# Optimization experiments

Measured on AMD Instinct MI355X. Metric: run time of the kernel, lower is better.

## Reference

```python
import jax, jax.numpy as jnp
import numpy as np
from jax import lax


def _fuse_proj(proj):
    # proj: [B,2,4,4] -> [B,4,4]; K @ [R|t] into top 3x4 of extrinsics
    p = proj[:, 0]
    new34 = jnp.einsum('bij,bjk->bik', proj[:, 1, :3, :3], proj[:, 0, :3, :4])
    return p.at[:, :3, :4].set(new34)


def _homo_warp(src_fea, src_proj, ref_proj, depth_values):
    # src_fea [B,C,H,W], src_proj/ref_proj [B,4,4], depth_values [B,D]
    B, C, H, W = src_fea.shape
    D = depth_values.shape[1]
    proj = jnp.einsum('bij,bjk->bik', src_proj, jnp.linalg.inv(ref_proj))
    rot, trans = proj[:, :3, :3], proj[:, :3, 3:4]
    y, x = jnp.meshgrid(jnp.arange(H, dtype=src_fea.dtype),
                        jnp.arange(W, dtype=src_fea.dtype), indexing='ij')
    xyz = jnp.stack([x.ravel(), y.ravel(), jnp.ones(H * W, src_fea.dtype)])  # [3,HW]
    rot_xyz = jnp.einsum('bij,jk->bik', rot, xyz)                            # [B,3,HW]
    pxyz = rot_xyz[:, :, None, :] * depth_values[:, None, :, None] + trans[:, :, None, :]  # [B,3,D,HW]
    z = pxyz[:, 2]
    px = pxyz[:, 0] / z   # pixel coords (align_corners=True convention)
    py = pxyz[:, 1] / z
    # bilinear sample with zeros padding
    x0 = jnp.floor(px); y0 = jnp.floor(py)
    x1 = x0 + 1.0;      y1 = y0 + 1.0
    wx1 = px - x0; wx0 = 1.0 - wx1
    wy1 = py - y0; wy0 = 1.0 - wy1
    fea_flat = src_fea.reshape(B, C, H * W)

    def corner(xc, yc, w):
        valid = (xc >= 0) & (xc <= W - 1) & (yc >= 0) & (yc <= H - 1)
        idx = (jnp.clip(yc, 0, H - 1).astype(jnp.int32) * W
               + jnp.clip(xc, 0, W - 1).astype(jnp.int32)).reshape(B, -1)   # [B,D*HW]
        g = jax.vmap(lambda f, i: jnp.take(f, i, axis=1))(fea_flat, idx)    # [B,C,D*HW]
        return g * (w * valid.astype(w.dtype)).reshape(B, 1, -1)

    out = (corner(x0, y0, wx0 * wy0) + corner(x1, y0, wx1 * wy0)
           + corner(x0, y1, wx0 * wy1) + corner(x1, y1, wx1 * wy1))
    return out.reshape(B, C, D, H, W)


def _forward(features, proj_matrices, depth_values, reg_w, num_depth):
    N = features.shape[0]
    ref_fea = features[0]                      # [B,C,H,W]
    ref_proj = _fuse_proj(proj_matrices[:, 0])
    B, C, H, W = ref_fea.shape
    D = num_depth

    vol_sum = jnp.broadcast_to(ref_fea[:, :, None], (B, C, D, H, W))
    vol_sq = vol_sum ** 2
    for i in range(1, N):                      # small fixed view loop
        src_proj = _fuse_proj(proj_matrices[:, i])
        wv = _homo_warp(features[i], src_proj, ref_proj, depth_values)
        vol_sum = vol_sum + wv
        vol_sq = vol_sq + wv ** 2
    inv_n = 1.0 / N
    variance = vol_sq * inv_n - (vol_sum * inv_n) ** 2   # [B,C,D,H,W]

    # cost regularization: 3x3x3 conv C->1 (stand-in for external 3D CNN)
    cost = lax.conv_general_dilated(variance, reg_w, (1, 1, 1), 'SAME',
                                    dimension_numbers=('NCDHW', 'OIDHW', 'NCDHW'))[:, 0]  # [B,D,H,W]
    prob = jax.nn.softmax(cost, axis=1)
    depth = jnp.sum(prob * depth_values[:, :, None, None], axis=1)          # [B,H,W]

    # photometric confidence (no-grad block)
    p = lax.stop_gradient(prob)
    # 4*avg_pool3d(pad(prob,(1,2)) over depth, kernel (4,1,1)) == sliding sum of 4
    sum4 = lax.reduce_window(p, 0.0, lax.add, (1, 4, 1, 1), (1, 1, 1, 1),
                             ((0, 0), (1, 2), (0, 0), (0, 0)))
    didx = jnp.sum(p * jnp.arange(D, dtype=p.dtype)[None, :, None, None], axis=1)
    didx = jnp.clip(didx.astype(jnp.int32), 0, D - 1)                        # [B,H,W]
    conf = jnp.take_along_axis(sum4, didx[:, None], axis=1)[:, 0]            # [B,H,W]
    return depth, conf


def setup_inputs() -> dict:
    key = jax.random.key(0)
    k1, k2, k3 = jax.random.split(key, 3)
    N, B, C, H, W, D = 5, 1, 32, 128, 160, 48
    features = jax.random.normal(k1, (N, B, C, H, W), jnp.float32)
    eye = jnp.eye(4, dtype=jnp.float32)
    proj_matrices = eye + 0.01 * jax.random.normal(k2, (B, N, 2, 4, 4), jnp.float32)
    depth_values = jnp.broadcast_to(
        425.0 + 510.0 * jnp.arange(D, dtype=jnp.float32) / (D - 1), (B, D))
    reg_w = 0.05 * jax.random.normal(k3, (1, C, 3, 3, 3), jnp.float32)
    return {"features": features, "proj_matrices": proj_matrices,
            "depth_values": depth_values, "reg_w": reg_w, "num_depth": D}


def reference(features, proj_matrices, depth_values, reg_w, num_depth):
    return _forward(features, proj_matrices, depth_values, reg_w, num_depth)
```

## Files before the change

kernel.cpp:

```cpp
#include <hip/hip_runtime.h>

#define W_ 160
#define H_ 128
#define C_ 32
#define D_ 48
#define HW_ (H_*W_)
#define TX 16
#define TY 16
#define HPX 18
#define HPY 18
#define NHP (HPX*HPY)
#define NHPP 336
#define NT 21
#define DST 28

typedef _Float16 h8 __attribute__((ext_vector_type(8)));
typedef __fp16 fp16x2 __attribute__((ext_vector_type(2)));
typedef float f4 __attribute__((ext_vector_type(4)));

__device__ __forceinline__ _Float16 u2h(unsigned int u) {
    union { unsigned short s; _Float16 h; } x; x.s = (unsigned short)u; return x.h;
}
__device__ __forceinline__ unsigned int pkh2(float a, float b) {
    union { fp16x2 h; unsigned int u; } x;
    x.h = __builtin_amdgcn_cvt_pkrtz(a, b);
    return x.u;
}

__device__ __forceinline__ void inv4x4(const float* a, float* inv) {
    inv[0]  =  a[5]*a[10]*a[15] - a[5]*a[11]*a[14] - a[9]*a[6]*a[15] + a[9]*a[7]*a[14] + a[13]*a[6]*a[11] - a[13]*a[7]*a[10];
    inv[4]  = -a[4]*a[10]*a[15] + a[4]*a[11]*a[14] + a[8]*a[6]*a[15] - a[8]*a[7]*a[14] - a[12]*a[6]*a[11] + a[12]*a[7]*a[10];
    inv[8]  =  a[4]*a[9]*a[15]  - a[4]*a[11]*a[13] - a[8]*a[5]*a[15] + a[8]*a[7]*a[13] + a[12]*a[5]*a[11] - a[12]*a[7]*a[9];
    inv[12] = -a[4]*a[9]*a[14]  + a[4]*a[10]*a[13] + a[8]*a[5]*a[14] - a[8]*a[6]*a[13] - a[12]*a[5]*a[10] + a[12]*a[6]*a[9];
    inv[1]  = -a[1]*a[10]*a[15] + a[1]*a[11]*a[14] + a[9]*a[2]*a[15] - a[9]*a[3]*a[14] - a[13]*a[2]*a[11] + a[13]*a[3]*a[10];
    inv[5]  =  a[0]*a[10]*a[15] - a[0]*a[11]*a[14] - a[8]*a[2]*a[15] + a[8]*a[3]*a[14] + a[12]*a[2]*a[11] - a[12]*a[3]*a[10];
    inv[9]  = -a[0]*a[9]*a[15]  + a[0]*a[11]*a[13] + a[8]*a[1]*a[15] - a[8]*a[3]*a[13] - a[12]*a[1]*a[11] + a[12]*a[3]*a[9];
    inv[13] =  a[0]*a[9]*a[14]  - a[0]*a[10]*a[13] - a[8]*a[1]*a[14] + a[8]*a[2]*a[13] + a[12]*a[1]*a[10] - a[12]*a[2]*a[9];
    inv[2]  =  a[1]*a[6]*a[15]  - a[1]*a[7]*a[14]  - a[5]*a[2]*a[15] + a[5]*a[3]*a[14] + a[13]*a[2]*a[7]  - a[13]*a[3]*a[6];
    inv[6]  = -a[0]*a[6]*a[15]  + a[0]*a[7]*a[14]  + a[4]*a[2]*a[15] - a[4]*a[3]*a[14] - a[12]*a[2]*a[7]  + a[12]*a[3]*a[6];
    inv[10] =  a[0]*a[5]*a[15]  - a[0]*a[7]*a[13]  - a[4]*a[1]*a[15] + a[4]*a[3]*a[13] + a[12]*a[1]*a[7]  - a[12]*a[3]*a[5];
    inv[14] = -a[0]*a[5]*a[14]  + a[0]*a[6]*a[13]  + a[4]*a[1]*a[14] - a[4]*a[2]*a[13] - a[12]*a[1]*a[6]  + a[12]*a[2]*a[5];
    inv[3]  = -a[1]*a[6]*a[11]  + a[1]*a[7]*a[10]  + a[5]*a[2]*a[11] - a[5]*a[3]*a[10] - a[9]*a[2]*a[7]   + a[9]*a[3]*a[6];
    inv[7]  =  a[0]*a[6]*a[11]  - a[0]*a[7]*a[10]  - a[4]*a[2]*a[11] + a[4]*a[3]*a[10] + a[8]*a[2]*a[7]   - a[8]*a[3]*a[6];
    inv[11] = -a[0]*a[5]*a[11]  + a[0]*a[7]*a[9]   + a[4]*a[1]*a[11] - a[4]*a[3]*a[9]  - a[8]*a[1]*a[7]   + a[8]*a[3]*a[5];
    inv[15] =  a[0]*a[5]*a[10]  - a[0]*a[6]*a[9]   - a[4]*a[1]*a[10] + a[4]*a[2]*a[9]  + a[8]*a[1]*a[6]   - a[8]*a[2]*a[5];
    float det = a[0]*inv[0] + a[1]*inv[4] + a[2]*inv[8] + a[3]*inv[12];
    float id = 1.0f / det;
    for (int i = 0; i < 16; ++i) inv[i] *= id;
}

__device__ __forceinline__ void fuseProj(const float* proj, int i, float* F) {
    const float* A = proj + i*32;
    const float* R = A + 16;
    for (int r = 0; r < 3; ++r)
        for (int k = 0; k < 4; ++k)
            F[r*4+k] = R[r*4]*A[k] + R[r*4+1]*A[4+k] + R[r*4+2]*A[8+k];
    for (int k = 0; k < 4; ++k) F[12+k] = A[12+k];
}

__global__ __launch_bounds__(256) void kS(const float* __restrict__ f,
                                          const float* __restrict__ proj,
                                          _Float16* __restrict__ ft,
                                          float* __restrict__ RX,
                                          float* __restrict__ M) {
    __shared__ float t[64][33];
    const int bx = blockIdx.x, v = blockIdx.y;
    const int tid = threadIdx.x;
    if (bx < 320) {
        const int p0 = bx * 64;
        const int pl = tid & 63;
        const int cb = (tid >> 6) * 8;
        #pragma unroll
        for (int k = 0; k < 8; ++k)
            t[pl][cb + k] = f[(size_t)(v*C_ + cb + k)*HW_ + p0 + pl];
        __syncthreads();
        const int px = tid >> 2;
        const int c0 = (tid & 3) * 8;
        h8 o;
        #pragma unroll
        for (int k = 0; k < 8; ++k) o[k] = (_Float16)t[px][c0 + k];
        *(h8*)&ft[((size_t)(v*HW_ + p0 + px) << 5) + c0] = o;
    } else {
        if (v >= 4) return;
        float F0[16], Fv[16], inv[16], P[12];
        fuseProj(proj, 0, F0);
        fuseProj(proj, v + 1, Fv);
        inv4x4(F0, inv);
        #pragma unroll
        for (int r = 0; r < 3; ++r)
            #pragma unroll
            for (int c = 0; c < 4; ++c) {
                float acc = 0.f;
                #pragma unroll
                for (int k = 0; k < 4; ++k) acc += Fv[r*4+k]*inv[k*4+c];
                P[r*4+c] = acc;
            }
        const int p = (bx - 320)*256 + tid;
        const float x = (float)(p % W_), y = (float)(p / W_);
        float4 o;
        o.x = P[0]*x + P[1]*y + P[2];
        o.y = P[4]*x + P[5]*y + P[6];
        o.z = P[8]*x + P[9]*y + P[10];
        o.w = 0.f;
        ((float4*)RX)[(size_t)v*HW_ + p] = o;
        if (bx == 320 && tid == 0) {
            float* om = M + v*12;
            om[0]=P[0]; om[1]=P[1]; om[2]=P[2];
            om[3]=P[4]; om[4]=P[5]; om[5]=P[6];
            om[6]=P[8]; om[7]=P[9]; om[8]=P[10];
            om[9]=P[3]; om[10]=P[7]; om[11]=P[11];
        }
    }
}

__global__ __launch_bounds__(256) void kA(const _Float16* __restrict__ featH,
                                          const float* __restrict__ RX,
                                          const float* __restrict__ M,
                                          const float* __restrict__ dvals,
                                          const float* __restrict__ regw,
                                          float* __restrict__ Q) {
    __shared__ __align__(16) _Float16 DL0[NHPP*DST];
    __shared__ __align__(16) _Float16 DL1[NHPP*DST];

    const int tid = threadIdx.x;
    const int bx = blockIdx.x, by = blockIdx.y;
    const int d0 = blockIdx.z*2, d1 = d0 + 1;
    const int lane = tid & 63;
    const int wv = tid >> 6;
    const int n = lane & 15;
    const int grp = lane >> 4;
    const float dv0 = dvals[d0], dv1 = dvals[d1];
    const float tx = M[grp*12 + 9], ty = M[grp*12 + 10], tz = M[grp*12 + 11];

    h8 bf0, bf1;
    {
        const int kb = grp * 8;
        #pragma unroll
        for (int j = 0; j < 8; ++j) {
            const int ch = kb + j;
            bf0[j] = (_Float16)regw[ch*27 + n];
            bf1[j] = (_Float16)((n < 11) ? regw[ch*27 + 16 + n] : 0.f);
        }
    }

    const h8 hz = {(_Float16)0,(_Float16)0,(_Float16)0,(_Float16)0,
                   (_Float16)0,(_Float16)0,(_Float16)0,(_Float16)0};
    const h8* F = (const h8*)featH;
    const float4* RX4 = (const float4*)RX;
    const f4 fz = {0.f, 0.f, 0.f, 0.f};

    #pragma unroll 1
    for (int pass = 0; pass < 6; ++pass) {
        const int tile = pass*4 + wv;
        if (tile >= NT) continue;
        const int px = tile*16 + n;
        const int hx = px % HPX;
        const int hy = px / HPX;
        const int lx = bx*TX + hx - 1;
        const int ly = by*TY + hy - 1;
        const bool pok = (px < NHP) && (lx >= 0) && (lx < W_) && (ly >= 0) && (ly < H_);
        const int rp = pok ? (ly*W_ + lx) : 0;

        unsigned pidx, pwax, pway, pwbx, pwby;
        {
            const float4 a = RX4[(size_t)grp*HW_ + rp];
            const float z0 = a.z*dv0 + tz;
            const float rz0 = 1.0f / z0;
            const float pxf0 = fminf(fmaxf((a.x*dv0 + tx)*rz0, -8.f), 168.f);
            const float pyf0 = fminf(fmaxf((a.y*dv0 + ty)*rz0, -8.f), 136.f);
            const float fx = floorf(pxf0), fy = floorf(pyf0);
            const float mxl = (fx >= 0.f  && fx <= 159.f) ? 1.f : 0.f;
            const float mxh = (fx >= -1.f && fx <= 158.f) ? 1.f : 0.f;
            const float myl = (fy >= 0.f  && fy <= 127.f) ? 1.f : 0.f;
            const float myh = (fy >= -1.f && fy <= 126.f) ? 1.f : 0.f;
            const int xs = (int)fminf(fmaxf(fx + 1.f, 0.f), 160.f);
            const int ys = (int)fminf(fmaxf(fy + 1.f, 0.f), 128.f);
            const int x0 = max(xs-1, 0), x1 = min(xs, W_-1);
            const int y0 = max(ys-1, 0), y1 = min(ys, H_-1);
            pidx = (unsigned)x0 | ((unsigned)x1 << 8)
                 | ((unsigned)y0 << 16) | ((unsigned)y1 << 24);
            const float wx1a = pxf0 - fx, wy1a = pyf0 - fy;
            pwax = pkh2((1.f - wx1a)*mxl, wx1a*mxh);
            pway = pkh2((1.f - wy1a)*myl, wy1a*myh);
            const float z1 = a.z*dv1 + tz;
            const float rz1 = 1.0f / z1;
            const float pxf1 = fminf(fmaxf((a.x*dv1 + tx)*rz1, -8.f), 168.f);
            const float pyf1 = fminf(fmaxf((a.y*dv1 + ty)*rz1, -8.f), 136.f);
            const float wx1b = pxf1 - fx, wy1b = pyf1 - fy;
            pwbx = pkh2((1.f - wx1b)*mxl, wx1b*mxh);
            pwby = pkh2((1.f - wy1b)*myl, wy1b*myh);
            if (!pok) { pwax = 0u; pway = 0u; pwbx = 0u; pwby = 0u; }
        }

        h8 var0 = hz, var1 = hz;
        h8 s0 = hz, q0 = hz, s1 = hz, q1 = hz;
        if (pok) {
            const h8 fr = F[(size_t)rp*4 + grp];
            s0 = fr; q0 = fr*fr; s1 = fr; q1 = q0;
        }
        #pragma unroll 1
        for (int v = 0; v < 4; ++v) {
            const int src = v*16 + n;
            const unsigned idxv = (unsigned)__shfl((int)pidx, src, 64);
            const unsigned ax   = (unsigned)__shfl((int)pwax, src, 64);
            const unsigned ay   = (unsigned)__shfl((int)pway, src, 64);
            const unsigned bxw  = (unsigned)__shfl((int)pwbx, src, 64);
            const unsigned byw  = (unsigned)__shfl((int)pwby, src, 64);
            if (pok) {
                const int x0 = idxv & 0xff, x1 = (idxv >> 8) & 0xff;
                const int y0W = ((idxv >> 16) & 0xff) * W_;
                const int y1W = (idxv >> 24) * W_;
                const h8* Fv = F + (size_t)(v+1)*HW_*4;
                const h8 f00 = Fv[(size_t)(y0W+x0)*4 + grp];
                const h8 f10 = Fv[(size_t)(y0W+x1)*4 + grp];
                const h8 f01 = Fv[(size_t)(y1W+x0)*4 + grp];
                const h8 f11 = Fv[(size_t)(y1W+x1)*4 + grp];
                const _Float16 wx0a = u2h(ax), wx1a = u2h(ax >> 16);
                const _Float16 wy0a = u2h(ay), wy1a = u2h(ay >> 16);
                const h8 g0 = f00*(wx0a*wy0a) + f10*(wx1a*wy0a)
                            + f01*(wx0a*wy1a) + f11*(wx1a*wy1a);
                s0 += g0; q0 += g0*g0;
                const _Float16 wx0b = u2h(bxw), wx1b = u2h(bxw >> 16);
                const _Float16 wy0b = u2h(byw), wy1b = u2h(byw >> 16);
                const h8 g1 = f00*(wx0b*wy0b) + f10*(wx1b*wy0b)
                            + f01*(wx0b*wy1b) + f11*(wx1b*wy1b);
                s1 += g1; q1 += g1*g1;
            }
        }
        if (pok) {
            const _Float16 c5 = (_Float16)0.2f;
            const h8 sa = s0 * c5, sb = s1 * c5;
            var0 = q0*c5 - sa*sa;
            var1 = q1*c5 - sb*sb;
        }
        const f4 a0 = __builtin_amdgcn_mfma_f32_16x16x32_f16(var0, bf0, fz, 0, 0, 0);
        const f4 b0 = __builtin_amdgcn_mfma_f32_16x16x32_f16(var0, bf1, fz, 0, 0, 0);
        const f4 a1 = __builtin_amdgcn_mfma_f32_16x16x32_f16(var1, bf0, fz, 0, 0, 0);
        const f4 b1 = __builtin_amdgcn_mfma_f32_16x16x32_f16(var1, bf1, fz, 0, 0, 0);
        const int rbase = tile*16 + grp*4;
        #pragma unroll
        for (int r = 0; r < 4; ++r) {
            _Float16* dr0 = &DL0[(rbase + r)*DST];
            _Float16* dr1 = &DL1[(rbase + r)*DST];
            dr0[n] = (_Float16)a0[r];
            dr1[n] = (_Float16)a1[r];
            if (n < 11) {
                dr0[16 + n] = (_Float16)b0[r];
                dr1[16 + n] = (_Float16)b1[r];
            }
        }
    }
    __syncthreads();

    {
        const int x = tid & 15;
        const int y = tid >> 4;
        float c00 = 0.f, c01 = 0.f, c02 = 0.f;
        float c10 = 0.f, c11 = 0.f, c12 = 0.f;
        #pragma unroll
        for (int jy = 0; jy < 3; ++jy) {
            #pragma unroll
            for (int jx = 0; jx < 3; ++jx) {
                const int hp = (y + jy)*HPX + (x + jx);
                const int sp = jy*3 + jx;
                const _Float16* dr0 = &DL0[hp*DST];
                const _Float16* dr1 = &DL1[hp*DST];
                c00 += (float)dr0[sp];
                c01 += (float)dr0[9 + sp];
                c02 += (float)dr0[18 + sp];
                c10 += (float)dr1[sp];
                c11 += (float)dr1[9 + sp];
                c12 += (float)dr1[18 + sp];
            }
        }
        const int p = (by*TY + y)*W_ + bx*TX + x;
        Q[(size_t)(0*D_ + d0)*HW_ + p] = c00;
        Q[(size_t)(1*D_ + d0)*HW_ + p] = c01;
        Q[(size_t)(2*D_ + d0)*HW_ + p] = c02;
        Q[(size_t)(0*D_ + d1)*HW_ + p] = c10;
        Q[(size_t)(1*D_ + d1)*HW_ + p] = c11;
        Q[(size_t)(2*D_ + d1)*HW_ + p] = c12;
    }
}

__global__ __launch_bounds__(64) void kB(const float* __restrict__ Q,
                                         const float* __restrict__ dvals,
                                         float* __restrict__ out) {
    const int p = blockIdx.x*64 + threadIdx.x;
    const float* Q0 = Q;
    const float* Q1 = Q + (size_t)D_*HW_;
    const float* Q2 = Q + (size_t)2*D_*HW_;
    float pr[D_];
    #pragma unroll
    for (int d = 0; d < D_; ++d) {
        float c = Q1[d*HW_ + p];
        if (d > 0)     c += Q0[(d-1)*HW_ + p];
        if (d < D_-1)  c += Q2[(d+1)*HW_ + p];
        pr[d] = c;
    }
    float m = pr[0];
    #pragma unroll
    for (int d = 1; d < D_; ++d) m = fmaxf(m, pr[d]);
    float s = 0.f;
    #pragma unroll
    for (int d = 0; d < D_; ++d) { const float e = __expf(pr[d] - m); pr[d] = e; s += e; }
    const float is = 1.f / s;
    float depth = 0.f, fidx = 0.f;
    #pragma unroll
    for (int d = 0; d < D_; ++d) {
        const float pp = pr[d] * is;
        pr[d] = pp;
        depth += pp * dvals[d];
        fidx  += pp * (float)d;
    }
    int di = (int)fidx;
    di = di < 0 ? 0 : (di > D_-1 ? D_-1 : di);
    float conf = 0.f;
    #pragma unroll
    for (int d = 0; d < D_; ++d)
        conf += ((d >= di-1) && (d <= di+2)) ? pr[d] : 0.f;
    out[p] = depth;
    out[HW_ + p] = conf;
}

extern "C" void kernel_launch(void* const* d_in, const int* in_sizes, int n_in,
                              void* d_out, int out_size, void* d_ws, size_t ws_size,
                              hipStream_t stream) {
    const float* features = (const float*)d_in[0];
    const float* proj     = (const float*)d_in[1];
    const float* dvals    = (const float*)d_in[2];
    const float* regw     = (const float*)d_in[3];
    float* out = (float*)d_out;

    _Float16* featH = (_Float16*)d_ws;
    float* RX = (float*)(featH + (size_t)5*HW_*C_);
    float* M  = RX + (size_t)4*HW_*4;
    float* Q  = M + 64;

    kS<<<dim3(400, 5), 256, 0, stream>>>(features, proj, featH, RX, M);
    kA<<<dim3(W_/TX, H_/TY, D_/2), 256, 0, stream>>>(featH, RX, M, dvals, regw, Q);
    kB<<<HW_/64, 64, 0, stream>>>(Q, dvals, out);
}
```

Baseline: 148.0 us.

## Scatter conv partial products via LDS float atomics instead of staged fp16 gather

Replaces the per-halo-pixel fp16 staging buffer (27 taps per pixel) and the 9-tap gather reduction with a compact float accumulator tile. Each MFMA output is atomically added into its target output-pixel slot in shared memory. This shrinks LDS per block from about 36KB to about 10KB, which the launch_bounds hint of 8 blocks per SM builds on, and keeps accumulation in fp32. In exchange it pays for many LDS atomic adds with possible contention, an extra zero-init pass, and an extra barrier.

Result: slower. 298.6 us (+101.8%).

```diff
diff --git a/kernel.cpp b/kernel.cpp
--- a/kernel.cpp
+++ b/kernel.cpp
@@ -10,9 +10,9 @@
 #define HPX 18
 #define HPY 18
 #define NHP (HPX*HPY)
-#define NHPP 336
 #define NT 21
-#define DST 28
+#define OSW 21
+#define OSN (20*OSW*3)
 
 typedef _Float16 h8 __attribute__((ext_vector_type(8)));
 typedef __fp16 fp16x2 __attribute__((ext_vector_type(2)));
@@ -113,14 +113,14 @@
     }
 }
 
-__global__ __launch_bounds__(256) void kA(const _Float16* __restrict__ featH,
-                                          const float* __restrict__ RX,
-                                          const float* __restrict__ M,
-                                          const float* __restrict__ dvals,
-                                          const float* __restrict__ regw,
-                                          float* __restrict__ Q) {
-    __shared__ __align__(16) _Float16 DL0[NHPP*DST];
-    __shared__ __align__(16) _Float16 DL1[NHPP*DST];
+__global__ __launch_bounds__(256, 8) void kA(const _Float16* __restrict__ featH,
+                                             const float* __restrict__ RX,
+                                             const float* __restrict__ M,
+                                             const float* __restrict__ dvals,
+                                             const float* __restrict__ regw,
+                                             float* __restrict__ Q) {
+    __shared__ float OS0[OSN];
+    __shared__ float OS1[OSN];
 
     const int tid = threadIdx.x;
     const int bx = blockIdx.x, by = blockIdx.y;
@@ -132,6 +132,8 @@
     const float dv0 = dvals[d0], dv1 = dvals[d1];
     const float tx = M[grp*12 + 9], ty = M[grp*12 + 10], tz = M[grp*12 + 11];
 
+    for (int i = tid; i < OSN; i += 256) { OS0[i] = 0.f; OS1[i] = 0.f; }
+
     h8 bf0, bf1;
     {
         const int kb = grp * 8;
@@ -142,6 +144,14 @@
             bf1[j] = (_Float16)((n < 11) ? regw[ch*27 + 16 + n] : 0.f);
         }
     }
+
+    const int kda = n / 9,        spa = n - kda*9;
+    const int Ka  = ((2 - spa/3)*OSW + (2 - spa%3))*3 + kda;
+    const int cb2 = 16 + n;
+    const int kdb = cb2 / 9,      spb = cb2 - kdb*9;
+    const int Kb  = ((2 - spb/3)*OSW + (2 - spb%3))*3 + kdb;
+
+    __syncthreads();
 
     const h8 hz = {(_Float16)0,(_Float16)0,(_Float16)0,(_Float16)0,
                    (_Float16)0,(_Float16)0,(_Float16)0,(_Float16)0};
@@ -154,10 +164,10 @@
         const int tile = pass*4 + wv;
         if (tile >= NT) continue;
         const int px = tile*16 + n;
-        const int hx = px % HPX;
-        const int hy = px / HPX;
-        const int lx = bx*TX + hx - 1;
-        const int ly = by*TY + hy - 1;
+        const int hx0 = px % HPX;
+        const int hy0 = px / HPX;
+        const int lx = bx*TX + hx0 - 1;
+        const int ly = by*TY + hy0 - 1;
         const bool pok = (px < NHP) && (lx >= 0) && (lx < W_) && (ly >= 0) && (ly < H_);
         const int rp = pok ? (ly*W_ + lx) : 0;
 
@@ -237,16 +247,20 @@
         const f4 b0 = __builtin_amdgcn_mfma_f32_16x16x32_f16(var0, bf1, fz, 0, 0, 0);
         const f4 a1 = __builtin_amdgcn_mfma_f32_16x16x32_f16(var1, bf0, fz, 0, 0, 0);
         const f4 b1 = __builtin_amdgcn_mfma_f32_16x16x32_f16(var1, bf1, fz, 0, 0, 0);
-        const int rbase = tile*16 + grp*4;
+        const int hpb = tile*16 + grp*4;
         #pragma unroll
         for (int r = 0; r < 4; ++r) {
-            _Float16* dr0 = &DL0[(rbase + r)*DST];
-            _Float16* dr1 = &DL1[(rbase + r)*DST];
-            dr0[n] = (_Float16)a0[r];
-            dr1[n] = (_Float16)a1[r];
-            if (n < 11) {
-                dr0[16 + n] = (_Float16)b0[r];
-                dr1[16 + n] = (_Float16)b1[r];
+            const int hp = hpb + r;
+            if (hp < NHP) {
+                const int hy = hp / HPX;
+                const int hx = hp - hy*HPX;
+                const int b3 = (hy*OSW + hx)*3;
+                atomicAdd(&OS0[b3 + Ka], a0[r]);
+                atomicAdd(&OS1[b3 + Ka], a1[r]);
+                if (n < 11) {
+                    atomicAdd(&OS0[b3 + Kb], b0[r]);
+                    atomicAdd(&OS1[b3 + Kb], b1[r]);
+                }
             }
         }
     }
@@ -255,31 +269,14 @@
     {
         const int x = tid & 15;
         const int y = tid >> 4;
-        float c00 = 0.f, c01 = 0.f, c02 = 0.f;
-        float c10 = 0.f, c11 = 0.f, c12 = 0.f;
-        #pragma unroll
-        for (int jy = 0; jy < 3; ++jy) {
-            #pragma unroll
-            for (int jx = 0; jx < 3; ++jx) {
-                const int hp = (y + jy)*HPX + (x + jx);
-                const int sp = jy*3 + jx;
-                const _Float16* dr0 = &DL0[hp*DST];
-                const _Float16* dr1 = &DL1[hp*DST];
-                c00 += (float)dr0[sp];
-                c01 += (float)dr0[9 + sp];
-                c02 += (float)dr0[18 + sp];
-                c10 += (float)dr1[sp];
-                c11 += (float)dr1[9 + sp];
-                c12 += (float)dr1[18 + sp];
-            }
-        }
+        const int cb3 = ((y + 2)*OSW + (x + 2))*3;
         const int p = (by*TY + y)*W_ + bx*TX + x;
-        Q[(size_t)(0*D_ + d0)*HW_ + p] = c00;
-        Q[(size_t)(1*D_ + d0)*HW_ + p] = c01;
-        Q[(size_t)(2*D_ + d0)*HW_ + p] = c02;
-        Q[(size_t)(0*D_ + d1)*HW_ + p] = c10;
-        Q[(size_t)(1*D_ + d1)*HW_ + p] = c11;
-        Q[(size_t)(2*D_ + d1)*HW_ + p] = c12;
+        Q[(size_t)(0*D_ + d0)*HW_ + p] = OS0[cb3 + 0];
+        Q[(size_t)(1*D_ + d0)*HW_ + p] = OS0[cb3 + 1];
+        Q[(size_t)(2*D_ + d0)*HW_ + p] = OS0[cb3 + 2];
+        Q[(size_t)(0*D_ + d1)*HW_ + p] = OS1[cb3 + 0];
+        Q[(size_t)(1*D_ + d1)*HW_ + p] = OS1[cb3 + 1];
+        Q[(size_t)(2*D_ + d1)*HW_ + p] = OS1[cb3 + 2];
     }
 }
 
```
